# Performance work log

Measured on AMD Instinct MI355X. Metric: run time of the kernel, lower is better.

Reference implementation:

```python
import jax, jax.numpy as jnp
import numpy as np

EPS = 1e-12  # matches torch F.normalize default eps


def _idx(k, pad, stride, size):
    o = (size + 2 * pad - k) // stride + 1
    return (jnp.arange(o) * stride)[:, None] + jnp.arange(k)[None, :], o  # [o, k]


def unfold(x, k, pad, stride):
    # x: [B, C, H, W] -> [B, C*k*k, oh*ow], torch F.unfold ordering (c slowest, then kh, kw)
    B, C, H, W = x.shape
    xp = jnp.pad(x, ((0, 0), (0, 0), (pad, pad), (pad, pad)))
    ri, oh = _idx(k, pad, stride, H)
    ci, ow = _idx(k, pad, stride, W)
    p = xp[:, :, ri[:, None, :, None], ci[None, :, None, :]]  # [B, C, oh, ow, k, k]
    return p.transpose(0, 1, 4, 5, 2, 3).reshape(B, C * k * k, oh * ow)


def fold(cols, out_hw, k, pad, stride):
    # inverse of unfold with overlap-add (torch F.fold)
    B, CKK, L = cols.shape
    C = CKK // (k * k)
    H, W = out_hw
    ri, oh = _idx(k, pad, stride, H)
    ci, ow = _idx(k, pad, stride, W)
    p = cols.reshape(B, C, k, k, oh, ow).transpose(0, 1, 4, 5, 2, 3)  # [B,C,oh,ow,k,k]
    canvas = jnp.zeros((B, C, H + 2 * pad, W + 2 * pad), cols.dtype)
    canvas = canvas.at[:, :, ri[:, None, :, None], ci[None, :, None, :]].add(p)
    return canvas[:, :, pad:pad + H, pad:pad + W]


def _l2norm(x, axis):
    n = jnp.sqrt(jnp.sum(x * x, axis=axis, keepdims=True))
    return x / jnp.maximum(n, EPS)


def setup_inputs() -> dict:
    key = jax.random.key(0)
    ks = jax.random.split(key, 5)
    return {
        "lrsr_lv3": jax.random.normal(ks[0], (1, 256, 48, 48), jnp.float32),
        "refsr_lv3": jax.random.normal(ks[1], (1, 256, 48, 48), jnp.float32),
        "ref_lv1": jax.random.normal(ks[2], (1, 64, 192, 192), jnp.float32),
        "ref_lv2": jax.random.normal(ks[3], (1, 128, 96, 96), jnp.float32),
        "ref_lv3": jax.random.normal(ks[4], (1, 256, 48, 48), jnp.float32),
    }


def reference(lrsr_lv3, refsr_lv3, ref_lv1, ref_lv2, ref_lv3):
    B, C, H, W = lrsr_lv3.shape
    lr_u = unfold(lrsr_lv3, 3, 1, 1)              # [B, C*9, L_lr]
    rf_u = unfold(refsr_lv3, 3, 1, 1)             # [B, C*9, L_ref]
    rf_n = _l2norm(rf_u.transpose(0, 2, 1), 2)    # [B, L_ref, C*9]
    lr_n = _l2norm(lr_u, 1)                       # [B, C*9, L_lr]
    R = jnp.einsum('brc,bcl->brl', rf_n, lr_n)    # [B, L_ref, L_lr] cosine corr
    R_star = jnp.max(R, axis=1)                   # [B, L_lr]
    R_arg = jnp.argmax(R, axis=1)                 # [B, L_lr]

    ref3_u = unfold(ref_lv3, 3, 1, 1)             # [B, C*9,   L_ref]
    ref2_u = unfold(ref_lv2, 6, 2, 2)             # [B, C2*36, L_ref]
    ref1_u = unfold(ref_lv1, 12, 4, 4)            # [B, C1*144,L_ref]

    idx = R_arg[:, None, :]                       # [B, 1, L_lr]
    T3_u = jnp.take_along_axis(ref3_u, idx, axis=2)
    T2_u = jnp.take_along_axis(ref2_u, idx, axis=2)
    T1_u = jnp.take_along_axis(ref1_u, idx, axis=2)

    T_lv3 = fold(T3_u, (H, W), 3, 1, 1) / 9.0
    T_lv2 = fold(T2_u, (H * 2, W * 2), 6, 2, 2) / 9.0
    T_lv1 = fold(T1_u, (H * 4, W * 4), 12, 4, 4) / 9.0
    S = R_star.reshape(B, 1, H, W)
    return (S, T_lv3, T_lv2, T_lv1)
```

## Files before the change

### kernel.cpp

```cpp
#include <hip/hip_runtime.h>
#include <hip/hip_bf16.h>
#include <math.h>

#define HW 48
#define NPOS 2304
#define CCH 256
#define PCOLS 2500
#define PLANESZ (NPOS * CCH)
#define KC 16
#define TM 128
#define TN 64

typedef __attribute__((ext_vector_type(8))) short short8v;
typedef __attribute__((ext_vector_type(16))) float f32x16;

__device__ inline void ph_ss2(int vb, const float* __restrict__ lr,
                              const float* __restrict__ ref, float* __restrict__ SS2,
                              float (*red)[64]) {
    const int img = vb / 36, bx = vb % 36;
    const float* imgp = img ? ref : lr;
    const int t = threadIdx.x;
    const int px = t & 63, cg = t >> 6;
    const int p = bx * 64 + px;
    const float* base = imgp + (size_t)cg * 64 * NPOS + p;
    float s = 0.f;
#pragma unroll 4
    for (int cc = 0; cc < 64; ++cc) {
        float v = base[(size_t)cc * NPOS];
        s = fmaf(v, v, s);
    }
    red[cg][px] = s;
    __syncthreads();
    if (cg == 0)
        SS2[img * NPOS + p] = red[0][px] + red[1][px] + red[2][px] + red[3][px];
}

__device__ inline void ph_split(int local, const float* __restrict__ lr,
                                const float* __restrict__ ref, ushort* __restrict__ planes) {
    const int img = local / 288;
    const int gid = (local % 288) * 256 + threadIdx.x;
    const float* src = img ? ref : lr;
    const int lane = gid & 63;
    const int k16  = (gid >> 6) & 15;
    const int blk  = gid >> 10;
    const int pos  = blk * 32 + (lane & 31);
    const int c0   = k16 * 16 + (lane >> 5) * 8;
    ushort h8[8], m8[8], l8[8];
#pragma unroll
    for (int e = 0; e < 8; ++e) {
        float a = src[(size_t)(c0 + e) * NPOS + pos];
        __hip_bfloat16 hb = __float2bfloat16(a);
        float hf = __bfloat162float(hb);
        float r1 = a - hf;
        __hip_bfloat16 mb = __float2bfloat16(r1);
        float mf = __bfloat162float(mb);
        __hip_bfloat16 lb = __float2bfloat16(r1 - mf);
        h8[e] = *(ushort*)&hb;
        m8[e] = *(ushort*)&mb;
        l8[e] = *(ushort*)&lb;
    }
    ushort* ph = planes + (size_t)(img * 3 + 0) * PLANESZ + (size_t)gid * 8;
    ushort* pm = planes + (size_t)(img * 3 + 1) * PLANESZ + (size_t)gid * 8;
    ushort* pl = planes + (size_t)(img * 3 + 2) * PLANESZ + (size_t)gid * 8;
#pragma unroll
    for (int e = 0; e < 8; ++e) { ph[e] = h8[e]; pm[e] = m8[e]; pl[e] = l8[e]; }
}

__device__ inline void ph_zero(int local, float* __restrict__ P) {
    const int idx = local * 256 + threadIdx.x;
    if (idx >= NPOS * 196) return;
    const int row = idx / 196, b = idx - row * 196;
    int pc;
    if (b < 50)       pc = b;
    else if (b < 100) pc = 2450 + (b - 50);
    else {
        const int i = b - 100;
        const int rr = 1 + (i >> 1);
        pc = rr * 50 + ((i & 1) ? 49 : 0);
    }
    P[(size_t)row * PCOLS + pc] = 0.f;
}

__device__ inline void ph_transpose(int b, const float* __restrict__ ref1,
                                    const float* __restrict__ ref2,
                                    const float* __restrict__ ref3,
                                    float* __restrict__ T3t, float* __restrict__ T2t,
                                    float* __restrict__ T1t, float (*tile)[65]) {
    const float* src; float* dst; int C, NPIX, tpx, tch;
    if (b < 144)      { src = ref3; dst = T3t; C = 256; NPIX = 2304;  tpx = b % 36;  tch = b / 36; }
    else if (b < 432) { const int lb = b - 144; src = ref2; dst = T2t; C = 128; NPIX = 9216;  tpx = lb % 144; tch = lb / 144; }
    else              { const int lb = b - 432; src = ref1; dst = T1t; C = 64;  NPIX = 36864; tpx = lb;       tch = 0; }
    const int t = threadIdx.x;
    const int px0 = tpx * 64, c0 = tch * 64;
#pragma unroll
    for (int r = 0; r < 16; ++r) {
        const int cl = r * 4 + (t >> 6), pl = t & 63;
        tile[cl][pl] = src[(size_t)(c0 + cl) * NPIX + px0 + pl];
    }
    __syncthreads();
#pragma unroll
    for (int r = 0; r < 16; ++r) {
        const int pl = r * 4 + (t >> 6), cl = t & 63;
        dst[(size_t)(px0 + pl) * C + c0 + cl] = tile[cl][pl];
    }
}

__global__ __launch_bounds__(256) void prep_kernel(const float* __restrict__ lr,
                                                   const float* __restrict__ ref,
                                                   const float* __restrict__ ref1,
                                                   const float* __restrict__ ref2,
                                                   const float* __restrict__ ref3,
                                                   float* __restrict__ SS2,
                                                   ushort* __restrict__ planes,
                                                   float* __restrict__ P,
                                                   float* __restrict__ T3t,
                                                   float* __restrict__ T2t,
                                                   float* __restrict__ T1t,
                                                   int do_split, int tbase) {
    __shared__ union {
        float red[4][64];
        float tile[64][65];
    } sm;
    const int b = blockIdx.x;
    if (b >= tbase) {
        ph_transpose(b - tbase, ref1, ref2, ref3, T3t, T2t, T1t, sm.tile);
        return;
    }
    if (do_split) {
        if (b < 72)        ph_ss2(b, lr, ref, SS2, sm.red);
        else if (b < 648)  ph_split(b - 72, lr, ref, planes);
        else               ph_zero(b - 648, P);
    } else {
        if (b < 72)        ph_ss2(b, lr, ref, SS2, sm.red);
        else               ph_zero(b - 72, P);
    }
}

__global__ __launch_bounds__(256) void transposeT_kernel(const float* __restrict__ ref1,
                                                         const float* __restrict__ ref2,
                                                         const float* __restrict__ ref3,
                                                         float* __restrict__ T3t,
                                                         float* __restrict__ T2t,
                                                         float* __restrict__ T1t) {
    __shared__ float tile[64][65];
    ph_transpose(blockIdx.x, ref1, ref2, ref3, T3t, T2t, T1t, tile);
}

__device__ inline void ph_invnorm(int vb, const float* __restrict__ SS2,
                                  float* __restrict__ inv2) {
    const int img = vb / 9;
    const int p = (vb % 9) * 256 + threadIdx.x;
    const float* SS = SS2 + img * NPOS;
    const int y = p / HW, x = p % HW;
    float s = 0.f;
#pragma unroll
    for (int di = -1; di <= 1; ++di) {
        int yy = y + di;
        if ((unsigned)yy >= HW) continue;
#pragma unroll
        for (int dj = -1; dj <= 1; ++dj) {
            int xx = x + dj;
            if ((unsigned)xx >= HW) continue;
            s += SS[yy * HW + xx];
        }
    }
    inv2[img * NPOS + p] = 1.f / fmaxf(sqrtf(s), 1e-12f);
}

__device__ inline void ph_gemm(int g, const ushort* __restrict__ planes,
                               float* __restrict__ P) {
    const int bxg = g % 72, byg = g / 72;
    const int t = threadIdx.x, lane = t & 63, w = t >> 6;
    const int nblk0 = bxg;
    const int ablk  = byg * 4 + w;

    const ushort* baseA  = planes + ((size_t)(ablk * 16) * 64 + lane) * 8;
    const ushort* baseB0 = planes + (size_t)3 * PLANESZ + ((size_t)(nblk0 * 16) * 64 + lane) * 8;

    f32x16 acc0 = {};
#pragma unroll 4
    for (int k = 0; k < 16; ++k) {
        const int fo = k * 512;
        short8v ah = *(const short8v*)(baseA + fo);
        short8v am = *(const short8v*)(baseA + PLANESZ + fo);
        short8v al = *(const short8v*)(baseA + 2 * PLANESZ + fo);
        short8v bh0 = *(const short8v*)(baseB0 + fo);
        short8v bm0 = *(const short8v*)(baseB0 + PLANESZ + fo);
        short8v bl0 = *(const short8v*)(baseB0 + 2 * PLANESZ + fo);
        acc0 = __builtin_amdgcn_mfma_f32_32x32x16_bf16(ah, bh0, acc0, 0, 0, 0);
        acc0 = __builtin_amdgcn_mfma_f32_32x32x16_bf16(ah, bm0, acc0, 0, 0, 0);
        acc0 = __builtin_amdgcn_mfma_f32_32x32x16_bf16(am, bh0, acc0, 0, 0, 0);
        acc0 = __builtin_amdgcn_mfma_f32_32x32x16_bf16(ah, bl0, acc0, 0, 0, 0);
        acc0 = __builtin_amdgcn_mfma_f32_32x32x16_bf16(al, bh0, acc0, 0, 0, 0);
        acc0 = __builtin_amdgcn_mfma_f32_32x32x16_bf16(am, bm0, acc0, 0, 0, 0);
    }
    const int m0 = byg * 128 + w * 32;
    const int half = lane >> 5;
    const int colA = nblk0 * 32 + (lane & 31);
    const int pcA = (colA / 48) * 50 + colA % 48 + 51;
#pragma unroll
    for (int r = 0; r < 16; ++r) {
        const int row = (r & 3) + 8 * (r >> 2) + 4 * half;
        P[(size_t)(m0 + row) * PCOLS + pcA] = acc0[r];
    }
}

__global__ __launch_bounds__(256) void corr_kernel(const float* __restrict__ SS2,
                                                   float* __restrict__ inv2,
                                                   const ushort* __restrict__ planes,
                                                   float* __restrict__ P,
                                                   int do_gemm) {
    const int b = blockIdx.x;
    if (b < 18)          ph_invnorm(b, SS2, inv2);
    else if (do_gemm)    ph_gemm(b - 18, planes, P);
}

__global__ __launch_bounds__(256) void gemm_p_kernel(const float* __restrict__ lr,
                                                     const float* __restrict__ ref,
                                                     float* __restrict__ P) {
    __shared__ float As[KC][TM];
    __shared__ float Bs[KC][TN];
    const int t  = threadIdx.x;
    const int tx = t & 15, ty = t >> 4;
    const int lp0 = blockIdx.y * TM, rp0 = blockIdx.x * TN;
    const int ac0 = t >> 5,        acol0 = (t & 31) << 2;
    const int ac1 = (t + 256) >> 5, acol1 = acol0;
    const int bc = t >> 4, bcol = (t & 15) << 2;
    float acc[8][4] = {};
    for (int c0 = 0; c0 < CCH; c0 += KC) {
        float4 a0 = *(const float4*)(lr  + (size_t)(c0 + ac0) * NPOS + lp0 + acol0);
        float4 a1 = *(const float4*)(lr  + (size_t)(c0 + ac1) * NPOS + lp0 + acol1);
        float4 b0 = *(const float4*)(ref + (size_t)(c0 + bc)  * NPOS + rp0 + bcol);
        __syncthreads();
        *(float4*)&As[ac0][acol0] = a0;
        *(float4*)&As[ac1][acol1] = a1;
        *(float4*)&Bs[bc][bcol]   = b0;
        __syncthreads();
#pragma unroll
        for (int kk = 0; kk < KC; ++kk) {
            float4 aA = *(const float4*)&As[kk][ty * 8];
            float4 aB = *(const float4*)&As[kk][ty * 8 + 4];
            float4 bb = *(const float4*)&Bs[kk][tx * 4];
            const float av[8] = {aA.x, aA.y, aA.z, aA.w, aB.x, aB.y, aB.z, aB.w};
            const float bv[4] = {bb.x, bb.y, bb.z, bb.w};
#pragma unroll
            for (int i = 0; i < 8; ++i)
#pragma unroll
                for (int j = 0; j < 4; ++j)
                    acc[i][j] = fmaf(av[i], bv[j], acc[i][j]);
        }
    }
    const int col0 = rp0 + tx * 4;
    const int pc0  = (col0 / 48) * 50 + (col0 % 48) + 51;
#pragma unroll
    for (int i = 0; i < 8; ++i) {
        const int m = lp0 + ty * 8 + i;
        float4 v = make_float4(acc[i][0], acc[i][1], acc[i][2], acc[i][3]);
        __builtin_memcpy(P + (size_t)m * PCOLS + pc0, &v, 16);
    }
}

__global__ __launch_bounds__(192) void maxarg_kernel(const float* __restrict__ P,
                                                     const float* __restrict__ inr,
                                                     const float* __restrict__ inl,
                                                     float* __restrict__ S,
                                                     int* __restrict__ arg) {
    const int bid = blockIdx.x;
    const int l   = (bid & 7) * 288 + (bid >> 3);
    const int yl = l / HW, xl = l % HW;
    const int t  = threadIdx.x;

    bool vmask[9];
    const float* bp[9];
#pragma unroll
    for (int d = 0; d < 9; ++d) {
        const int di = d / 3 - 1, dj = d % 3 - 1;
        vmask[d] = ((unsigned)(yl + di) < HW) && ((unsigned)(xl + dj) < HW);
        bp[d] = P + (ptrdiff_t)(l + di * HW + dj) * PCOLS + (di * 50 + dj);
    }

    float best = -1e30f;
    int bestr = 0;
#pragma unroll
    for (int vv = 0; vv < 3; ++vv) {
        const int v   = t + vv * 192;
        const int yr  = v / 12;
        const int xr4 = (v - yr * 12) << 2;
        const int q0  = yr * 50 + xr4 + 51;
        const int r0  = yr * HW + xr4;
        float4 a = make_float4(0.f, 0.f, 0.f, 0.f);
#pragma unroll
        for (int d = 0; d < 9; ++d) {
            if (vmask[d]) {
                float4 x;
                __builtin_memcpy(&x, bp[d] + q0, 16);
                a.x += x.x; a.y += x.y; a.z += x.z; a.w += x.w;
            }
        }
        const float4 w = *(const float4*)(inr + r0);
        const float vals[4] = {a.x * w.x, a.y * w.y, a.z * w.z, a.w * w.w};
#pragma unroll
        for (int k = 0; k < 4; ++k)
            if (vals[k] > best) { best = vals[k]; bestr = r0 + k; }
    }

    __shared__ float bv[256];
    __shared__ int   br[256];
    bv[t] = best; br[t] = bestr;
    if (t < 64) { bv[192 + t] = -1e30f; br[192 + t] = 0; }
    __syncthreads();
    for (int s2 = 128; s2 > 0; s2 >>= 1) {
        if (t < s2) {
            float v2 = bv[t + s2]; int r2 = br[t + s2];
            if (v2 > bv[t] || (v2 == bv[t] && r2 < br[t])) { bv[t] = v2; br[t] = r2; }
        }
        __syncthreads();
    }
    if (t == 0) {
        S[l]   = bv[0] * inl[l];
        arg[l] = br[0];
    }
}

template <int S_, int C, int H>
__device__ inline void foldT(const float* __restrict__ refT, const int* __restrict__ arg,
                             float* __restrict__ out, int u, int lane) {
    const int y = u / 48, m = u % 48;
    const int ty_ = y / S_ + 1;
    float4 acc = make_float4(0.f, 0.f, 0.f, 0.f);
#pragma unroll
    for (int a = 0; a < 3; ++a) {
        const int oy = ty_ - a;
        if ((unsigned)oy >= HW) continue;
        const int di = y + S_ - S_ * oy;
#pragma unroll
        for (int b = 0; b < 3; ++b) {
            const int ox = m + 1 - b;
            if ((unsigned)ox >= HW) continue;
            const int ar = arg[oy * HW + ox];
            const int ry = ar / HW, rx = ar % HW;
            const int yy  = S_ * ry + di - S_;
            const int xx0 = S_ * (rx + b - 1);
            if ((unsigned)yy < H && (unsigned)xx0 < H) {
                float4 v;
                __builtin_memcpy(&v, refT + ((size_t)yy * H + xx0) * C + lane * 4, 16);
                acc.x += v.x; acc.y += v.y; acc.z += v.z; acc.w += v.w;
            }
        }
    }
    const int idx = lane * 4;
    const int xx = idx / C;
    const int c  = idx % C;
    const int x  = m * S_ + xx;
    const float vals[4] = {acc.x, acc.y, acc.z, acc.w};
    float* op = out + (size_t)c * (H * H) + (size_t)y * H + x;
#pragma unroll
    for (int e = 0; e < 4; ++e)
        op[(size_t)e * (H * H)] = vals[e] * (1.f / 9.f);
}

__global__ __launch_bounds__(256) void foldT_kernel(const float* __restrict__ T1t,
                                                    const float* __restrict__ T2t,
                                                    const float* __restrict__ T3t,
                                                    const int* __restrict__ argb,
                                                    float* __restrict__ T1,
                                                    float* __restrict__ T2,
                                                    float* __restrict__ T3) {
    const int b = blockIdx.x, w = threadIdx.x >> 6, lane = threadIdx.x & 63;
    if (b < 576)        foldT<1, 256, 48>(T3t, argb, T3, b * 4 + w, lane);
    else if (b < 1728)  foldT<2, 128, 96>(T2t, argb, T2, (b - 576) * 4 + w, lane);
    else                foldT<4, 64, 192>(T1t, argb, T1, (b - 1728) * 4 + w, lane);
}

extern "C" void kernel_launch(void* const* d_in, const int* in_sizes, int n_in,
                              void* d_out, int out_size, void* d_ws, size_t ws_size,
                              hipStream_t stream) {
    const float* lrsr  = (const float*)d_in[0];
    const float* refsr = (const float*)d_in[1];
    const float* ref1  = (const float*)d_in[2];
    const float* ref2  = (const float*)d_in[3];
    const float* ref3  = (const float*)d_in[4];

    float* out = (float*)d_out;
    float* S   = out;
    float* T3  = S  + NPOS;
    float* T2  = T3 + 256 * 48 * 48;
    float* T1  = T2 + 128 * 96 * 96;

    float*  P      = (float*)d_ws;
    float*  SS2    = P + (size_t)NPOS * PCOLS;
    float*  inv2   = SS2 + 2 * NPOS;
    int*    argb   = (int*)(inv2 + 2 * NPOS);
    ushort* planes = (ushort*)(argb + NPOS);
    float*  inl    = inv2;
    float*  inr    = inv2 + NPOS;

    const size_t need  = ((size_t)NPOS * PCOLS + 5 * NPOS) * 4 + (size_t)6 * PLANESZ * 2;
    const size_t nhwcB = (size_t)(2304 * 256 + 9216 * 128 + 36864 * 64) * 4;
    const int mfma_path = ws_size >= need ? 1 : 0;
    const int bigws     = ws_size >= need + nhwcB ? 1 : 0;

    float* T3t = bigws ? (float*)((char*)d_ws + need) : P;
    float* T2t = T3t + 2304 * 256;
    float* T1t = T2t + 9216 * 128;

    {
        const int tbase = mfma_path ? 2412 : 1836;
        const int grid  = tbase + (bigws ? 1008 : 0);
        prep_kernel<<<grid, 256, 0, stream>>>(lrsr, refsr, ref1, ref2, ref3,
                                              SS2, planes, P, T3t, T2t, T1t,
                                              mfma_path, bigws ? tbase : grid + 1);
    }

    if (mfma_path) {
        corr_kernel<<<18 + 1296, 256, 0, stream>>>(SS2, inv2, planes, P, 1);
    } else {
        corr_kernel<<<18, 256, 0, stream>>>(SS2, inv2, planes, P, 0);
        gemm_p_kernel<<<dim3(NPOS / TN, NPOS / TM), 256, 0, stream>>>(lrsr, refsr, P);
    }

    maxarg_kernel<<<NPOS, 192, 0, stream>>>(P, inr, inl, S, argb);

    if (!bigws)
        transposeT_kernel<<<1008, 256, 0, stream>>>(ref1, ref2, ref3, T3t, T2t, T1t);

    foldT_kernel<<<4032, 256, 0, stream>>>(T1t, T2t, T3t, argb, T1, T2, T3);
}
```

Measured before the change: 81.54 us.

## Process two adjacent LR positions per maxarg block and add nontemporal loads/stores

Each maxarg block now computes the 3x3 diagonal-sum correlation for two horizontally adjacent LR positions. The shared middle columns of the P matrix are loaded once and reused for both outputs, which halves the grid and cuts redundant global reads. Nontemporal loads are added in the transpose phase and nontemporal stores in the fold output, to reduce cache pollution. The cost is more registers per thread, a second reduction in shared memory, and some unaligned float4 loads.

```diff
diff --git a/kernel.cpp b/kernel.cpp
--- a/kernel.cpp
+++ b/kernel.cpp
@@ -95,7 +95,7 @@
 #pragma unroll
     for (int r = 0; r < 16; ++r) {
         const int cl = r * 4 + (t >> 6), pl = t & 63;
-        tile[cl][pl] = src[(size_t)(c0 + cl) * NPIX + px0 + pl];
+        tile[cl][pl] = __builtin_nontemporal_load(&src[(size_t)(c0 + cl) * NPIX + px0 + pl]);
     }
     __syncthreads();
 #pragma unroll
@@ -266,21 +266,23 @@
                                                      float* __restrict__ S,
                                                      int* __restrict__ arg) {
     const int bid = blockIdx.x;
-    const int l   = (bid & 7) * 288 + (bid >> 3);
-    const int yl = l / HW, xl = l % HW;
-    const int t  = threadIdx.x;
-
-    bool vmask[9];
-    const float* bp[9];
-#pragma unroll
-    for (int d = 0; d < 9; ++d) {
-        const int di = d / 3 - 1, dj = d % 3 - 1;
-        vmask[d] = ((unsigned)(yl + di) < HW) && ((unsigned)(xl + dj) < HW);
-        bp[d] = P + (ptrdiff_t)(l + di * HW + dj) * PCOLS + (di * 50 + dj);
-    }
-
-    float best = -1e30f;
-    int bestr = 0;
+    const int pl  = (bid & 7) * 144 + (bid >> 3);
+    const int yl  = pl / 24, xl0 = (pl % 24) * 2;
+    const int l0  = yl * HW + xl0;
+    const int t   = threadIdx.x;
+
+    bool vrow[3][4];
+    const float* rp[3][4];
+#pragma unroll
+    for (int di = -1; di <= 1; ++di)
+#pragma unroll
+        for (int j = -1; j <= 2; ++j) {
+            vrow[di + 1][j + 1] = ((unsigned)(yl + di) < HW) && ((unsigned)(xl0 + j) < HW);
+            rp[di + 1][j + 1]   = P + (ptrdiff_t)(l0 + di * HW + j) * PCOLS + (di * 50 + j);
+        }
+
+    float best0 = -1e30f, best1 = -1e30f;
+    int bestr0 = 0, bestr1 = 0;
 #pragma unroll
     for (int vv = 0; vv < 3; ++vv) {
         const int v   = t + vv * 192;
@@ -288,37 +290,64 @@
         const int xr4 = (v - yr * 12) << 2;
         const int q0  = yr * 50 + xr4 + 51;
         const int r0  = yr * HW + xr4;
-        float4 a = make_float4(0.f, 0.f, 0.f, 0.f);
-#pragma unroll
-        for (int d = 0; d < 9; ++d) {
-            if (vmask[d]) {
+        float4 a0 = make_float4(0.f, 0.f, 0.f, 0.f);
+        float4 a1 = make_float4(0.f, 0.f, 0.f, 0.f);
+#pragma unroll
+        for (int di = 0; di < 3; ++di) {
+            if (vrow[di][0]) {
                 float4 x;
-                __builtin_memcpy(&x, bp[d] + q0, 16);
-                a.x += x.x; a.y += x.y; a.z += x.z; a.w += x.w;
+                __builtin_memcpy(&x, rp[di][0] + q0, 16);
+                a0.x += x.x; a0.y += x.y; a0.z += x.z; a0.w += x.w;
             }
+#pragma unroll
+            for (int j = 1; j <= 2; ++j) {
+                if (vrow[di][j]) {
+                    float4 x;
+                    __builtin_memcpy(&x, rp[di][j] + q0 - 1, 16);
+                    const float s = *(rp[di][j] + q0 + 3);
+                    a1.x += x.x; a1.y += x.y; a1.z += x.z; a1.w += x.w;
+                    a0.x += x.y; a0.y += x.z; a0.z += x.w; a0.w += s;
+                }
+            }
+            if (vrow[di][3]) {
+                float4 x;
+                __builtin_memcpy(&x, rp[di][3] + q0 - 1, 16);
+                a1.x += x.x; a1.y += x.y; a1.z += x.z; a1.w += x.w;
+            }
         }
         const float4 w = *(const float4*)(inr + r0);
-        const float vals[4] = {a.x * w.x, a.y * w.y, a.z * w.z, a.w * w.w};
-#pragma unroll
-        for (int k = 0; k < 4; ++k)
-            if (vals[k] > best) { best = vals[k]; bestr = r0 + k; }
-    }
-
-    __shared__ float bv[256];
-    __shared__ int   br[256];
-    bv[t] = best; br[t] = bestr;
-    if (t < 64) { bv[192 + t] = -1e30f; br[192 + t] = 0; }
+        const float v0[4] = {a0.x * w.x, a0.y * w.y, a0.z * w.z, a0.w * w.w};
+        const float v1[4] = {a1.x * w.x, a1.y * w.y, a1.z * w.z, a1.w * w.w};
+#pragma unroll
+        for (int k = 0; k < 4; ++k) {
+            if (v0[k] > best0) { best0 = v0[k]; bestr0 = r0 + k; }
+            if (v1[k] > best1) { best1 = v1[k]; bestr1 = r0 + k; }
+        }
+    }
+
+    __shared__ float bv0[256], bv1[256];
+    __shared__ int   br0[256], br1[256];
+    bv0[t] = best0; br0[t] = bestr0;
+    bv1[t] = best1; br1[t] = bestr1;
+    if (t < 64) {
+        bv0[192 + t] = -1e30f; br0[192 + t] = 0;
+        bv1[192 + t] = -1e30f; br1[192 + t] = 0;
+    }
     __syncthreads();
     for (int s2 = 128; s2 > 0; s2 >>= 1) {
         if (t < s2) {
-            float v2 = bv[t + s2]; int r2 = br[t + s2];
-            if (v2 > bv[t] || (v2 == bv[t] && r2 < br[t])) { bv[t] = v2; br[t] = r2; }
+            float x0 = bv0[t + s2]; int y0 = br0[t + s2];
+            if (x0 > bv0[t] || (x0 == bv0[t] && y0 < br0[t])) { bv0[t] = x0; br0[t] = y0; }
+            float x1 = bv1[t + s2]; int y1 = br1[t + s2];
+            if (x1 > bv1[t] || (x1 == bv1[t] && y1 < br1[t])) { bv1[t] = x1; br1[t] = y1; }
         }
         __syncthreads();
     }
     if (t == 0) {
-        S[l]   = bv[0] * inl[l];
-        arg[l] = br[0];
+        S[l0]     = bv0[0] * inl[l0];
+        arg[l0]   = br0[0];
+        S[l0 + 1] = bv1[0] * inl[l0 + 1];
+        arg[l0 + 1] = br1[0];
     }
 }
 
@@ -356,7 +385,7 @@
     float* op = out + (size_t)c * (H * H) + (size_t)y * H + x;
 #pragma unroll
     for (int e = 0; e < 4; ++e)
-        op[(size_t)e * (H * H)] = vals[e] * (1.f / 9.f);
+        __builtin_nontemporal_store(vals[e] * (1.f / 9.f), &op[(size_t)e * (H * H)]);
 }
 
 __global__ __launch_bounds__(256) void foldT_kernel(const float* __restrict__ T1t,
@@ -419,7 +448,7 @@
         gemm_p_kernel<<<dim3(NPOS / TN, NPOS / TM), 256, 0, stream>>>(lrsr, refsr, P);
     }
 
-    maxarg_kernel<<<NPOS, 192, 0, stream>>>(P, inr, inl, S, argb);
+    maxarg_kernel<<<1152, 192, 0, stream>>>(P, inr, inl, S, argb);
 
     if (!bigws)
         transposeT_kernel<<<1008, 256, 0, stream>>>(ref1, ref2, ref3, T3t, T2t, T1t);
```

Result: slower. 111.2 us (+36.4%).
